# Optimization experiments

Measured on AMD Instinct MI355X. Metric: run time of the kernel, lower is better.

## Reference

```python
import jax, jax.numpy as jnp
import numpy as np

B, N, FE, T, OUT = 32, 2048, 32, 12, 3


def setup_inputs() -> dict:
    key = jax.random.key(0)
    ks = jax.random.split(key, 7)
    return {
        "x": jax.random.normal(ks[0], (B, N, FE, T), dtype=jnp.float32),
        "w_ih": jax.random.normal(ks[1], (3, FE), dtype=jnp.float32) * 0.1,
        "w_hh": jax.random.normal(ks[2], (3, 1), dtype=jnp.float32) * 0.1,
        "b_ih": jax.random.normal(ks[3], (3,), dtype=jnp.float32) * 0.1,
        "b_hh": jax.random.normal(ks[4], (3,), dtype=jnp.float32) * 0.1,
        "lin_w": jax.random.normal(ks[5], (OUT, T), dtype=jnp.float32) * 0.1,
        "lin_b": jax.random.normal(ks[6], (OUT,), dtype=jnp.float32) * 0.1,
        "unused": 0,
    }


def reference(x, w_ih, w_hh, b_ih, b_hh, lin_w, lin_b, unused):
    b, n, fe, t = x.shape
    # [B,N,Fe,T] -> [M,T,Fe] with M = B*N
    xs = jnp.transpose(x.reshape(-1, fe, t), (0, 2, 1))
    # Precompute input-to-gate projections for all timesteps: [M,T,3] (r,z,n gates)
    gates_x = jnp.einsum("mtf,gf->mtg", xs, w_ih) + b_ih
    wh = w_hh[:, 0]  # [3] recurrent weights, hidden size is 1

    def step(h, gx):
        # h: [M], gx: [M,3]
        r = jax.nn.sigmoid(gx[:, 0] + wh[0] * h + b_hh[0])
        z = jax.nn.sigmoid(gx[:, 1] + wh[1] * h + b_hh[1])
        nn_ = jnp.tanh(gx[:, 2] + r * (wh[2] * h + b_hh[2]))
        h_new = (1.0 - z) * nn_ + z * h
        return h_new, h_new

    h0 = jnp.zeros(xs.shape[0], dtype=x.dtype)
    _, hs = jax.lax.scan(step, h0, jnp.swapaxes(gates_x, 0, 1))  # [T,M]
    h = jax.nn.relu(hs.T)  # [M,T] (squeeze of [M,T,1])
    out = h @ lin_w.T + lin_b  # [M,OUT]
    return out.reshape(b, n, -1)
```

## Files before the change

### kernel.cpp

```cpp
#include <hip/hip_runtime.h>

#define FE_ 32
#define T_  12
#define M_  (32 * 2048)
#define SEQ_PER_BLOCK 32
#define THREADS (SEQ_PER_BLOCK * T_)
#define LDS_STRIDE 37

__global__ __launch_bounds__(THREADS) void gru_fused_kernel(
    const float* __restrict__ x,
    const float* __restrict__ w_ih,
    const float* __restrict__ w_hh,
    const float* __restrict__ b_ih,
    const float* __restrict__ b_hh,
    const float* __restrict__ lin_w,
    const float* __restrict__ lin_b,
    float* __restrict__ out)
{
    __shared__ float gbuf[SEQ_PER_BLOCK * LDS_STRIDE];

    const int tid = threadIdx.x;
    const int s   = tid / T_;
    const int t   = tid - s * T_;
    const int m0  = blockIdx.x * SEQ_PER_BLOCK;

    const float* __restrict__ xp = x + (size_t)(m0 + s) * (FE_ * T_) + t;
    float a0 = b_ih[0], a1 = b_ih[1], a2 = b_ih[2];
#pragma unroll
    for (int f = 0; f < FE_; ++f) {
        const float xv = xp[f * T_];
        a0 = fmaf(xv, w_ih[0 * FE_ + f], a0);
        a1 = fmaf(xv, w_ih[1 * FE_ + f], a1);
        a2 = fmaf(xv, w_ih[2 * FE_ + f], a2);
    }
    float* g = &gbuf[s * LDS_STRIDE + t * 3];
    g[0] = a0; g[1] = a1; g[2] = a2;
    __syncthreads();

    if (tid < SEQ_PER_BLOCK) {
        const float wh0 = w_hh[0], wh1 = w_hh[1], wh2 = w_hh[2];
        const float bh0 = b_hh[0], bh1 = b_hh[1], bh2 = b_hh[2];
        float o0 = lin_b[0], o1 = lin_b[1], o2 = lin_b[2];
        const float* __restrict__ gg = &gbuf[tid * LDS_STRIDE];
        float h = 0.0f;
#pragma unroll
        for (int tt = 0; tt < T_; ++tt) {
            const float r = 1.0f / (1.0f + __expf(-(gg[tt * 3 + 0] + wh0 * h + bh0)));
            const float z = 1.0f / (1.0f + __expf(-(gg[tt * 3 + 1] + wh1 * h + bh1)));
            const float y = gg[tt * 3 + 2] + r * (wh2 * h + bh2);
            const float n = 1.0f - 2.0f / (1.0f + __expf(2.0f * y));
            h = (1.0f - z) * n + z * h;
            const float ht = h > 0.0f ? h : 0.0f;
            o0 = fmaf(ht, lin_w[0 * T_ + tt], o0);
            o1 = fmaf(ht, lin_w[1 * T_ + tt], o1);
            o2 = fmaf(ht, lin_w[2 * T_ + tt], o2);
        }
        float* __restrict__ po = out + (size_t)(m0 + tid) * 3;
        po[0] = o0; po[1] = o1; po[2] = o2;
    }
}

extern "C" void kernel_launch(void* const* d_in, const int* in_sizes, int n_in,
                              void* d_out, int out_size, void* d_ws, size_t ws_size,
                              hipStream_t stream) {
    (void)in_sizes; (void)n_in; (void)d_ws; (void)ws_size; (void)out_size;
    const float* x     = (const float*)d_in[0];
    const float* w_ih  = (const float*)d_in[1];
    const float* w_hh  = (const float*)d_in[2];
    const float* b_ih  = (const float*)d_in[3];
    const float* b_hh  = (const float*)d_in[4];
    const float* lin_w = (const float*)d_in[5];
    const float* lin_b = (const float*)d_in[6];
    float* out = (float*)d_out;

    const int grid = M_ / SEQ_PER_BLOCK;
    gru_fused_kernel<<<grid, THREADS, 0, stream>>>(x, w_ih, w_hh, b_ih, b_hh,
                                                   lin_w, lin_b, out);
}
```

Measured before the change: 159.1 us.

## Stage x tile through LDS with coalesced float4 loads, halve sequences per block

Each block now reads its 16 sequences of x (16×384 floats) from global memory as contiguous float4 loads into a padded shared-memory buffer. The per-timestep gate projection then reads from LDS instead of issuing strided scalar global loads. The block size drops from 32 to 16 sequences to keep the added LDS footprint moderate. This targets poor global load efficiency in the input projection, which is the dominant memory traffic, at the cost of extra LDS usage and an additional barrier.

```diff
diff --git a/kernel.cpp b/kernel.cpp
--- a/kernel.cpp
+++ b/kernel.cpp
@@ -3,9 +3,10 @@
 #define FE_ 32
 #define T_  12
 #define M_  (32 * 2048)
-#define SEQ_PER_BLOCK 32
-#define THREADS (SEQ_PER_BLOCK * T_)
-#define LDS_STRIDE 37
+#define SEQ 16
+#define THREADS (SEQ * T_)
+#define XSTR 392
+#define GSTR 37
 
 __global__ __launch_bounds__(THREADS) void gru_fused_kernel(
     const float* __restrict__ x,
@@ -17,31 +18,42 @@
     const float* __restrict__ lin_b,
     float* __restrict__ out)
 {
-    __shared__ float gbuf[SEQ_PER_BLOCK * LDS_STRIDE];
+    __shared__ float xs[SEQ * XSTR];
+    __shared__ float gbuf[SEQ * GSTR];
 
     const int tid = threadIdx.x;
-    const int s   = tid / T_;
-    const int t   = tid - s * T_;
-    const int m0  = blockIdx.x * SEQ_PER_BLOCK;
+    const int m0  = blockIdx.x * SEQ;
 
-    const float* __restrict__ xp = x + (size_t)(m0 + s) * (FE_ * T_) + t;
+    const float4* __restrict__ xg = (const float4*)(x + (size_t)m0 * (FE_ * T_));
+    const int sl = tid / 96;
+    const int rl = (tid - sl * 96) * 4;
+#pragma unroll
+    for (int i = 0; i < 8; ++i) {
+        const float4 v = xg[i * THREADS + tid];
+        *(float4*)&xs[(i * 2 + sl) * XSTR + rl] = v;
+    }
+    __syncthreads();
+
+    const int s = tid / T_;
+    const int t = tid - s * T_;
     float a0 = b_ih[0], a1 = b_ih[1], a2 = b_ih[2];
+    const float* __restrict__ xr = &xs[s * XSTR + t];
 #pragma unroll
     for (int f = 0; f < FE_; ++f) {
-        const float xv = xp[f * T_];
+        const float xv = xr[f * T_];
         a0 = fmaf(xv, w_ih[0 * FE_ + f], a0);
         a1 = fmaf(xv, w_ih[1 * FE_ + f], a1);
         a2 = fmaf(xv, w_ih[2 * FE_ + f], a2);
     }
-    float* g = &gbuf[s * LDS_STRIDE + t * 3];
+    float* g = &gbuf[s * GSTR + t * 3];
     g[0] = a0; g[1] = a1; g[2] = a2;
     __syncthreads();
 
-    if (tid < SEQ_PER_BLOCK) {
+    if (tid < SEQ) {
         const float wh0 = w_hh[0], wh1 = w_hh[1], wh2 = w_hh[2];
         const float bh0 = b_hh[0], bh1 = b_hh[1], bh2 = b_hh[2];
         float o0 = lin_b[0], o1 = lin_b[1], o2 = lin_b[2];
-        const float* __restrict__ gg = &gbuf[tid * LDS_STRIDE];
+        const float* __restrict__ gg = &gbuf[tid * GSTR];
         float h = 0.0f;
 #pragma unroll
         for (int tt = 0; tt < T_; ++tt) {
@@ -73,7 +85,7 @@
     const float* lin_b = (const float*)d_in[6];
     float* out = (float*)d_out;
 
-    const int grid = M_ / SEQ_PER_BLOCK;
+    const int grid = M_ / SEQ;
     gru_fused_kernel<<<grid, THREADS, 0, stream>>>(x, w_ih, w_hh, b_ih, b_hh,
                                                    lin_w, lin_b, out);
 }
```

After: 161.6 us. Within noise of the previous version (+1.6%).
